# Kernel optimization log

Hardware: AMD Instinct MI355X
Metric: run time of the kernel (lower is better)

## Reference

```python
import jax, jax.numpy as jnp
import numpy as np

B, P, D, T = 4096, 19000, 4000, 32
H1, H2 = 2048, 1024
DIN = 2 * P + 2


def setup_inputs() -> dict:
    key = jax.random.key(0)
    ks = jax.random.split(key, 9)
    drug_pairs = jax.random.randint(ks[0], (B, 2), 0, D)
    drug_targets = jax.random.randint(ks[1], (D, T), 0, P)
    conc = jax.random.uniform(ks[2], (B, 2), dtype=jnp.float32)
    s = lambda n: 1.0 / np.sqrt(n).astype(np.float32)
    W1 = jax.random.normal(ks[3], (DIN, H1), dtype=jnp.float32) * s(DIN)
    b1 = jnp.zeros((H1,), jnp.float32)
    W2 = jax.random.normal(ks[4], (H1, H2), dtype=jnp.float32) * s(H1)
    b2 = jnp.zeros((H2,), jnp.float32)
    W3 = jax.random.normal(ks[5], (H2, 1), dtype=jnp.float32) * s(H2)
    b3 = jnp.zeros((1,), jnp.float32)
    return {"drug_pairs": drug_pairs, "drug_targets": drug_targets, "conc": conc,
            "W1": W1, "b1": b1, "W2": W2, "b2": b2, "W3": W3, "b3": b3}


def _multi_hot(drug_ids, drug_targets):
    # drug_ids: [B]; gather per-drug target lists [B, T], scatter 1s into [B, P]
    tgt = drug_targets[drug_ids]  # [B, T]
    rows = jnp.arange(drug_ids.shape[0])[:, None]
    return jnp.zeros((drug_ids.shape[0], P), jnp.float32).at[rows, tgt].set(1.0)


def reference(drug_pairs, drug_targets, conc, W1, b1, W2, b2, W3, b3):
    prot_1 = _multi_hot(drug_pairs[:, 0], drug_targets)  # [B, P]
    prot_2 = _multi_hot(drug_pairs[:, 1], drug_targets)  # [B, P]
    data_1 = jnp.concatenate([prot_1, conc[:, 0:1]], axis=1)  # [B, P+1]
    data_2 = jnp.concatenate([prot_2, conc[:, 1:2]], axis=1)
    order_1 = jnp.concatenate([data_1, data_2], axis=1)  # [B, 2P+2]
    order_2 = jnp.concatenate([data_2, data_1], axis=1)

    def mlp(x):
        h = jax.nn.relu(x @ W1 + b1)
        h = jax.nn.relu(h @ W2 + b2)
        return h @ W3 + b3

    return (mlp(order_1)[:, 0], mlp(order_2)[:, 0])
```

## Files before the change

kernel.cpp:

```cpp
#include <hip/hip_runtime.h>
#include <stdint.h>

#define B_N  4096
#define P_N  19000
#define D_N  4000
#define T_N  32
#define H1_N 2048
#define H2_N 1024

typedef __bf16 bf16x8 __attribute__((ext_vector_type(8)));
typedef float  f32x4  __attribute__((ext_vector_type(4)));

__device__ __forceinline__ unsigned short f2bf(float f) {
  union { float f; uint32_t u; } v; v.f = f;
  uint32_t u = v.u;
  uint32_t r = (u + 0x7fffu + ((u >> 16) & 1u)) >> 16;
  return (unsigned short)r;
}

__device__ __forceinline__ float bflo(uint32_t u) {
  union { uint32_t u; float f; } v; v.u = u << 16; return v.f;
}
__device__ __forceinline__ float bfhi(uint32_t u) {
  union { uint32_t u; float f; } v; v.u = u & 0xffff0000u; return v.f;
}

__device__ __forceinline__ void gload16(const void* g, void* l) {
  __builtin_amdgcn_global_load_lds((const __attribute__((address_space(1))) void*)g,
                                   (__attribute__((address_space(3))) void*)l,
                                   16, 0, 0);
}

__global__ __launch_bounds__(256) void k_prep(const float* __restrict__ W1,
                                              unsigned short* __restrict__ W1b,
                                              const float* __restrict__ W2,
                                              unsigned short* __restrict__ W2T,
                                              const int* __restrict__ dp,
                                              unsigned char* __restrict__ flags) {
  __shared__ float tile[32][33];
  const int b = blockIdx.x;
  if (b < 38002) {
    const size_t base = (size_t)b * H1_N + threadIdx.x * 8;
    const float4* p = (const float4*)(W1 + base);
    float4 x = p[0], y = p[1];
    unsigned short r[8] = { f2bf(x.x), f2bf(x.y), f2bf(x.z), f2bf(x.w),
                            f2bf(y.x), f2bf(y.y), f2bf(y.z), f2bf(y.w) };
    *(uint4*)(W1b + base) = *(uint4*)r;
  } else if (b < 38002 + 2048) {
    const int bb = b - 38002;
    const int bx = bb & 31;
    const int by = bb >> 5;
    const int tx = threadIdx.x & 31, ty = threadIdx.x >> 5;
    #pragma unroll
    for (int i = 0; i < 4; ++i)
      tile[ty + i*8][tx] = W2[(size_t)(by*32 + ty + i*8) * H2_N + bx*32 + tx];
    __syncthreads();
    #pragma unroll
    for (int i = 0; i < 4; ++i) {
      const int n = bx*32 + ty + i*8;
      const int k = by*32 + tx;
      W2T[(size_t)n * H1_N + k] = f2bf(tile[tx][ty + i*8]);
    }
  } else {
    const int tid = threadIdx.x;
    for (int i = tid; i < D_N; i += 256) flags[i] = 0;
    __syncthreads();
    for (int i = tid; i < 2 * B_N; i += 256) flags[dp[i]] = 1;
  }
}

__global__ __launch_bounds__(256) void k_dsum(const int* __restrict__ dt,
                                              const unsigned char* __restrict__ flags,
                                              const unsigned short* __restrict__ W1b,
                                              unsigned short* __restrict__ SAb,
                                              unsigned short* __restrict__ SBb) {
  const int d = blockIdx.x;
  if (!flags[d]) return;
  __shared__ int   tgt[T_N];
  __shared__ float wgt[T_N];
  const int tid = threadIdx.x;
  if (tid < T_N) tgt[tid] = dt[d * T_N + tid];
  __syncthreads();
  if (tid < T_N) {
    int v = 1, t = tgt[tid];
    for (int j = 0; j < tid; ++j) v &= (tgt[j] != t);
    wgt[tid] = (float)v;
  }
  __syncthreads();
  const int c0 = tid * 8;
  float aA[8] = {0,0,0,0,0,0,0,0};
  float aB[8] = {0,0,0,0,0,0,0,0};
  #pragma unroll 4
  for (int t = 0; t < T_N; ++t) {
    const float  w   = wgt[t];
    const size_t row = (size_t)tgt[t];
    uint4 a = *(const uint4*)(W1b + row * H1_N + c0);
    uint4 b = *(const uint4*)(W1b + (19001 + row) * H1_N + c0);
    uint32_t au[4] = {a.x, a.y, a.z, a.w};
    uint32_t bu[4] = {b.x, b.y, b.z, b.w};
    #pragma unroll
    for (int k = 0; k < 4; ++k) {
      aA[2*k]   = fmaf(w, bflo(au[k]), aA[2*k]);
      aA[2*k+1] = fmaf(w, bfhi(au[k]), aA[2*k+1]);
      aB[2*k]   = fmaf(w, bflo(bu[k]), aB[2*k]);
      aB[2*k+1] = fmaf(w, bfhi(bu[k]), aB[2*k+1]);
    }
  }
  unsigned short oa[8], ob[8];
  #pragma unroll
  for (int k = 0; k < 8; ++k) { oa[k] = f2bf(aA[k]); ob[k] = f2bf(aB[k]); }
  *(uint4*)(SAb + (size_t)d * H1_N + c0) = *(uint4*)oa;
  *(uint4*)(SBb + (size_t)d * H1_N + c0) = *(uint4*)ob;
}

__global__ __launch_bounds__(256) void k_h1(const int* __restrict__ dp, const float* __restrict__ conc,
                                            const float* __restrict__ W1, const float* __restrict__ b1,
                                            const unsigned short* __restrict__ SAb,
                                            const unsigned short* __restrict__ SBb,
                                            unsigned short* __restrict__ h1) {
  const int rI   = blockIdx.x;
  const int swap = (rI >= B_N) ? 1 : 0;
  const int rr   = swap ? rI - B_N : rI;
  const int dA = dp[2*rr + swap];
  const int dB = dp[2*rr + (1 - swap)];
  const float cA = conc[2*rr + swap];
  const float cB = conc[2*rr + (1 - swap)];
  const int c0 = threadIdx.x * 8;
  uint4 ua = *(const uint4*)(SAb + (size_t)dA * H1_N + c0);
  uint4 ub = *(const uint4*)(SBb + (size_t)dB * H1_N + c0);
  uint32_t au[4] = {ua.x, ua.y, ua.z, ua.w};
  uint32_t bu[4] = {ub.x, ub.y, ub.z, ub.w};
  const float4* wp = (const float4*)(W1 + (size_t)P_N * H1_N + c0);
  const float4* wq = (const float4*)(W1 + (size_t)(2*P_N + 1) * H1_N + c0);
  const float4* bp = (const float4*)(b1 + c0);
  float a[8], b[8], p[8], q[8], z[8];
  #pragma unroll
  for (int k = 0; k < 4; ++k) {
    a[2*k] = bflo(au[k]); a[2*k+1] = bfhi(au[k]);
    b[2*k] = bflo(bu[k]); b[2*k+1] = bfhi(bu[k]);
  }
  float4 p0 = wp[0], p1 = wp[1], q0 = wq[0], q1 = wq[1], z0 = bp[0], z1 = bp[1];
  p[0]=p0.x;p[1]=p0.y;p[2]=p0.z;p[3]=p0.w;p[4]=p1.x;p[5]=p1.y;p[6]=p1.z;p[7]=p1.w;
  q[0]=q0.x;q[1]=q0.y;q[2]=q0.z;q[3]=q0.w;q[4]=q1.x;q[5]=q1.y;q[6]=q1.z;q[7]=q1.w;
  z[0]=z0.x;z[1]=z0.y;z[2]=z0.z;z[3]=z0.w;z[4]=z1.x;z[5]=z1.y;z[6]=z1.z;z[7]=z1.w;
  unsigned short res[8];
  #pragma unroll
  for (int k = 0; k < 8; ++k)
    res[k] = f2bf(fmaxf(a[k] + b[k] + cA*p[k] + cB*q[k] + z[k], 0.f));
  *(uint4*)(h1 + (size_t)rI * H1_N + c0) = *(uint4*)res;
}

__global__ __launch_bounds__(256, 2) void k_gemm(const unsigned short* __restrict__ A,
                                                 const unsigned short* __restrict__ Bm,
                                                 const float* __restrict__ b2,
                                                 const float* __restrict__ W3,
                                                 float* __restrict__ partial) {
  __shared__ unsigned short As[64 * 64];
  __shared__ unsigned short Bs[256 * 64];
  __shared__ float ps[4][64];
  const int tid  = threadIdx.x;
  const int wv   = tid >> 6;
  const int lane = tid & 63;
  const int bid  = blockIdx.x;
  const int m0 = (bid >> 2) * 64;
  const int nq = bid & 3;
  const int n0 = nq * 256;
  const int wn = wv * 64;
  const int r = lane & 15;
  const int g = lane >> 4;
  const int srow = lane >> 3;
  const int slot = (lane & 7) ^ srow;

  f32x4 acc[4][4] = {};

  for (int kt = 0; kt < 32; ++kt) {
    const int k0 = kt * 64;
    #pragma unroll
    for (int i = 0; i < 2; ++i) {
      const int c   = i * 4 + wv;
      const int row = c * 8 + srow;
      gload16(A + (size_t)(m0 + row) * H1_N + k0 + slot * 8, (char*)As + c * 1024);
    }
    #pragma unroll
    for (int i = 0; i < 8; ++i) {
      const int c   = i * 4 + wv;
      const int row = c * 8 + srow;
      gload16(Bm + (size_t)(n0 + row) * H1_N + k0 + slot * 8, (char*)Bs + c * 1024);
    }
    __syncthreads();
    #pragma unroll
    for (int kk = 0; kk < 2; ++kk) {
      bf16x8 af[4], bfr[4];
      #pragma unroll
      for (int mi = 0; mi < 4; ++mi) {
        const int row = mi * 16 + r;
        const int s   = (kk * 4 + g) ^ (row & 7);
        af[mi] = *(const bf16x8*)((const char*)As + row * 128 + s * 16);
      }
      #pragma unroll
      for (int ni = 0; ni < 4; ++ni) {
        const int col = wn + ni * 16 + r;
        const int s   = (kk * 4 + g) ^ (col & 7);
        bfr[ni] = *(const bf16x8*)((const char*)Bs + col * 128 + s * 16);
      }
      #pragma unroll
      for (int mi = 0; mi < 4; ++mi)
        #pragma unroll
        for (int ni = 0; ni < 4; ++ni)
          acc[mi][ni] = __builtin_amdgcn_mfma_f32_16x16x32_bf16(af[mi], bfr[ni], acc[mi][ni], 0, 0, 0);
    }
    __syncthreads();
  }
  float b2v[4], w3v[4];
  #pragma unroll
  for (int ni = 0; ni < 4; ++ni) {
    const int col = n0 + wn + ni * 16 + r;
    b2v[ni] = b2[col];
    w3v[ni] = W3[col];
  }
  float rs[16];
  #pragma unroll
  for (int mi = 0; mi < 4; ++mi)
    #pragma unroll
    for (int q = 0; q < 4; ++q) {
      float s = 0.f;
      #pragma unroll
      for (int ni = 0; ni < 4; ++ni)
        s += fmaxf(acc[mi][ni][q] + b2v[ni], 0.f) * w3v[ni];
      rs[mi*4+q] = s;
    }
  #pragma unroll
  for (int o = 1; o < 16; o <<= 1)
    #pragma unroll
    for (int k = 0; k < 16; ++k)
      rs[k] += __shfl_xor(rs[k], o, 64);
  if (r == 0)
    #pragma unroll
    for (int mi = 0; mi < 4; ++mi)
      #pragma unroll
      for (int q = 0; q < 4; ++q)
        ps[wv][mi*16 + g*4 + q] = rs[mi*4+q];
  __syncthreads();
  if (tid < 64)
    partial[(size_t)nq * (2*B_N) + m0 + tid] =
        ps[0][tid] + ps[1][tid] + ps[2][tid] + ps[3][tid];
}

__global__ __launch_bounds__(256) void k_fin(const float* __restrict__ partial,
                                             const float* __restrict__ b3,
                                             float* __restrict__ out) {
  const int i = blockIdx.x * 256 + threadIdx.x;
  float s = b3[0];
  #pragma unroll
  for (int j = 0; j < 4; ++j) s += partial[(size_t)j * (2*B_N) + i];
  out[i] = s;
}

extern "C" void kernel_launch(void* const* d_in, const int* in_sizes, int n_in,
                              void* d_out, int out_size, void* d_ws, size_t ws_size,
                              hipStream_t stream) {
  const int*   dp   = (const int*)d_in[0];
  const int*   dt   = (const int*)d_in[1];
  const float* conc = (const float*)d_in[2];
  const float* W1   = (const float*)d_in[3];
  const float* b1   = (const float*)d_in[4];
  const float* W2   = (const float*)d_in[5];
  const float* b2   = (const float*)d_in[6];
  const float* W3   = (const float*)d_in[7];
  const float* b3   = (const float*)d_in[8];
  float* out = (float*)d_out;

  char* ws = (char*)d_ws;
  unsigned short* W1b   = (unsigned short*)ws;
  unsigned short* h1    = (unsigned short*)ws;
  float*          parts = (float*)(ws + 33554432);
  unsigned short* SAb   = (unsigned short*)(ws + 155656192);
  unsigned short* SBb   = (unsigned short*)(ws + 172040192);
  unsigned short* w2t   = (unsigned short*)(ws + 188424192);
  unsigned char*  flags = (unsigned char*)(ws + 192618496);

  k_prep<<<40051,  256, 0, stream>>>(W1, W1b, W2, w2t, dp, flags);
  k_dsum<<<D_N,    256, 0, stream>>>(dt, flags, W1b, SAb, SBb);
  k_h1  <<<2*B_N,  256, 0, stream>>>(dp, conc, W1, b1, SAb, SBb, h1);
  k_gemm<<<512,    256, 0, stream>>>(h1, w2t, b2, W3, parts);
  k_fin <<<32,     256, 0, stream>>>(parts, b3, out);
}
```

Before: 267.8 us.

## Interleave paired W1 rows in bf16 copy and double-buffer GEMM LDS tiles

The bf16 conversion of W1 now converts only the 19000 protein rows used by the gather, storing row p of the first half and row 19001+p of the second half interleaved so k_dsum reads both with one contiguous 32-byte access per thread. This drops conversion of unused rows (the conc rows) and halves the prep block count. The layer-2 GEMM now double-buffers its A and B LDS tiles, issuing the next k-tile's global-to-LDS loads before computing on the current one, and reuses the A buffer for the final reduction scratch. LDS use roughly doubles, which may limit the two-blocks-per-CU occupancy.

```diff
diff --git a/kernel.cpp b/kernel.cpp
--- a/kernel.cpp
+++ b/kernel.cpp
@@ -32,22 +32,27 @@
 }
 
 __global__ __launch_bounds__(256) void k_prep(const float* __restrict__ W1,
-                                              unsigned short* __restrict__ W1b,
+                                              unsigned short* __restrict__ W1i,
                                               const float* __restrict__ W2,
                                               unsigned short* __restrict__ W2T,
                                               const int* __restrict__ dp,
                                               unsigned char* __restrict__ flags) {
   __shared__ float tile[32][33];
   const int b = blockIdx.x;
-  if (b < 38002) {
-    const size_t base = (size_t)b * H1_N + threadIdx.x * 8;
-    const float4* p = (const float4*)(W1 + base);
-    float4 x = p[0], y = p[1];
-    unsigned short r[8] = { f2bf(x.x), f2bf(x.y), f2bf(x.z), f2bf(x.w),
-                            f2bf(y.x), f2bf(y.y), f2bf(y.z), f2bf(y.w) };
-    *(uint4*)(W1b + base) = *(uint4*)r;
-  } else if (b < 38002 + 2048) {
-    const int bb = b - 38002;
+  if (b < 19000) {
+    const int tid = threadIdx.x;
+    const float4* pa = (const float4*)(W1 + (size_t)b * H1_N + tid * 8);
+    const float4* pb = (const float4*)(W1 + (size_t)(19001 + b) * H1_N + tid * 8);
+    float4 a0 = pa[0], a1 = pa[1], b0 = pb[0], b1 = pb[1];
+    unsigned short ra[8] = { f2bf(a0.x), f2bf(a0.y), f2bf(a0.z), f2bf(a0.w),
+                             f2bf(a1.x), f2bf(a1.y), f2bf(a1.z), f2bf(a1.w) };
+    unsigned short rb[8] = { f2bf(b0.x), f2bf(b0.y), f2bf(b0.z), f2bf(b0.w),
+                             f2bf(b1.x), f2bf(b1.y), f2bf(b1.z), f2bf(b1.w) };
+    unsigned short* dst = W1i + (size_t)b * 4096 + tid * 16;
+    *(uint4*)(dst)     = *(uint4*)ra;
+    *(uint4*)(dst + 8) = *(uint4*)rb;
+  } else if (b < 19000 + 2048) {
+    const int bb = b - 19000;
     const int bx = bb & 31;
     const int by = bb >> 5;
     const int tx = threadIdx.x & 31, ty = threadIdx.x >> 5;
@@ -71,7 +76,7 @@
 
 __global__ __launch_bounds__(256) void k_dsum(const int* __restrict__ dt,
                                               const unsigned char* __restrict__ flags,
-                                              const unsigned short* __restrict__ W1b,
+                                              const unsigned short* __restrict__ W1i,
                                               unsigned short* __restrict__ SAb,
                                               unsigned short* __restrict__ SBb) {
   const int d = blockIdx.x;
@@ -87,15 +92,14 @@
     wgt[tid] = (float)v;
   }
   __syncthreads();
-  const int c0 = tid * 8;
   float aA[8] = {0,0,0,0,0,0,0,0};
   float aB[8] = {0,0,0,0,0,0,0,0};
   #pragma unroll 4
   for (int t = 0; t < T_N; ++t) {
-    const float  w   = wgt[t];
-    const size_t row = (size_t)tgt[t];
-    uint4 a = *(const uint4*)(W1b + row * H1_N + c0);
-    uint4 b = *(const uint4*)(W1b + (19001 + row) * H1_N + c0);
+    const float w = wgt[t];
+    const uint4* pp = (const uint4*)(W1i + (size_t)tgt[t] * 4096 + tid * 16);
+    uint4 a = pp[0];
+    uint4 b = pp[1];
     uint32_t au[4] = {a.x, a.y, a.z, a.w};
     uint32_t bu[4] = {b.x, b.y, b.z, b.w};
     #pragma unroll
@@ -109,6 +113,7 @@
   unsigned short oa[8], ob[8];
   #pragma unroll
   for (int k = 0; k < 8; ++k) { oa[k] = f2bf(aA[k]); ob[k] = f2bf(aB[k]); }
+  const int c0 = tid * 8;
   *(uint4*)(SAb + (size_t)d * H1_N + c0) = *(uint4*)oa;
   *(uint4*)(SBb + (size_t)d * H1_N + c0) = *(uint4*)ob;
 }
@@ -155,9 +160,8 @@
                                                  const float* __restrict__ b2,
                                                  const float* __restrict__ W3,
                                                  float* __restrict__ partial) {
-  __shared__ unsigned short As[64 * 64];
-  __shared__ unsigned short Bs[256 * 64];
-  __shared__ float ps[4][64];
+  __shared__ unsigned short As[2][64 * 64];
+  __shared__ unsigned short Bs[2][256 * 64];
   const int tid  = threadIdx.x;
   const int wv   = tid >> 6;
   const int lane = tid & 63;
@@ -173,21 +177,41 @@
 
   f32x4 acc[4][4] = {};
 
-  for (int kt = 0; kt < 32; ++kt) {
-    const int k0 = kt * 64;
+  {
+    const int k0 = 0;
     #pragma unroll
     for (int i = 0; i < 2; ++i) {
       const int c   = i * 4 + wv;
       const int row = c * 8 + srow;
-      gload16(A + (size_t)(m0 + row) * H1_N + k0 + slot * 8, (char*)As + c * 1024);
+      gload16(A + (size_t)(m0 + row) * H1_N + k0 + slot * 8, (char*)As[0] + c * 1024);
     }
     #pragma unroll
     for (int i = 0; i < 8; ++i) {
       const int c   = i * 4 + wv;
       const int row = c * 8 + srow;
-      gload16(Bm + (size_t)(n0 + row) * H1_N + k0 + slot * 8, (char*)Bs + c * 1024);
-    }
-    __syncthreads();
+      gload16(Bm + (size_t)(n0 + row) * H1_N + k0 + slot * 8, (char*)Bs[0] + c * 1024);
+    }
+  }
+  __syncthreads();
+
+  for (int kt = 0; kt < 32; ++kt) {
+    const int cb = kt & 1;
+    if (kt < 31) {
+      const int k0 = (kt + 1) * 64;
+      const int nb = cb ^ 1;
+      #pragma unroll
+      for (int i = 0; i < 2; ++i) {
+        const int c   = i * 4 + wv;
+        const int row = c * 8 + srow;
+        gload16(A + (size_t)(m0 + row) * H1_N + k0 + slot * 8, (char*)As[nb] + c * 1024);
+      }
+      #pragma unroll
+      for (int i = 0; i < 8; ++i) {
+        const int c   = i * 4 + wv;
+        const int row = c * 8 + srow;
+        gload16(Bm + (size_t)(n0 + row) * H1_N + k0 + slot * 8, (char*)Bs[nb] + c * 1024);
+      }
+    }
     #pragma unroll
     for (int kk = 0; kk < 2; ++kk) {
       bf16x8 af[4], bfr[4];
@@ -195,13 +219,13 @@
       for (int mi = 0; mi < 4; ++mi) {
         const int row = mi * 16 + r;
         const int s   = (kk * 4 + g) ^ (row & 7);
-        af[mi] = *(const bf16x8*)((const char*)As + row * 128 + s * 16);
+        af[mi] = *(const bf16x8*)((const char*)As[cb] + row * 128 + s * 16);
       }
       #pragma unroll
       for (int ni = 0; ni < 4; ++ni) {
         const int col = wn + ni * 16 + r;
         const int s   = (kk * 4 + g) ^ (col & 7);
-        bfr[ni] = *(const bf16x8*)((const char*)Bs + col * 128 + s * 16);
+        bfr[ni] = *(const bf16x8*)((const char*)Bs[cb] + col * 128 + s * 16);
       }
       #pragma unroll
       for (int mi = 0; mi < 4; ++mi)
@@ -211,6 +235,7 @@
     }
     __syncthreads();
   }
+  float* ps = (float*)As;
   float b2v[4], w3v[4];
   #pragma unroll
   for (int ni = 0; ni < 4; ++ni) {
@@ -239,11 +264,11 @@
     for (int mi = 0; mi < 4; ++mi)
       #pragma unroll
       for (int q = 0; q < 4; ++q)
-        ps[wv][mi*16 + g*4 + q] = rs[mi*4+q];
+        ps[wv * 64 + mi*16 + g*4 + q] = rs[mi*4+q];
   __syncthreads();
   if (tid < 64)
     partial[(size_t)nq * (2*B_N) + m0 + tid] =
-        ps[0][tid] + ps[1][tid] + ps[2][tid] + ps[3][tid];
+        ps[0*64 + tid] + ps[1*64 + tid] + ps[2*64 + tid] + ps[3*64 + tid];
 }
 
 __global__ __launch_bounds__(256) void k_fin(const float* __restrict__ partial,
@@ -271,7 +296,7 @@
   float* out = (float*)d_out;
 
   char* ws = (char*)d_ws;
-  unsigned short* W1b   = (unsigned short*)ws;
+  unsigned short* W1i   = (unsigned short*)ws;
   unsigned short* h1    = (unsigned short*)ws;
   float*          parts = (float*)(ws + 33554432);
   unsigned short* SAb   = (unsigned short*)(ws + 155656192);
@@ -279,8 +304,8 @@
   unsigned short* w2t   = (unsigned short*)(ws + 188424192);
   unsigned char*  flags = (unsigned char*)(ws + 192618496);
 
-  k_prep<<<40051,  256, 0, stream>>>(W1, W1b, W2, w2t, dp, flags);
-  k_dsum<<<D_N,    256, 0, stream>>>(dt, flags, W1b, SAb, SBb);
+  k_prep<<<21049,  256, 0, stream>>>(W1, W1i, W2, w2t, dp, flags);
+  k_dsum<<<D_N,    256, 0, stream>>>(dt, flags, W1i, SAb, SBb);
   k_h1  <<<2*B_N,  256, 0, stream>>>(dp, conc, W1, b1, SAb, SBb, h1);
   k_gemm<<<512,    256, 0, stream>>>(h1, w2t, b2, W3, parts);
   k_fin <<<32,     256, 0, stream>>>(parts, b3, out);
```

Result: slower. 290.0 us (+8.3%).
